# Kernel tuning notes

Hardware: AMD Instinct MI355X
Metric: run time of the kernel (lower is better)

Reference implementation:

```python
import jax, jax.numpy as jnp
import numpy as np

B, S, N = 1, 128, 256
C_IN, C_H, C_OUT = 256, 32, 128
EPS = 1e-5


def setup_inputs() -> dict:
    key = jax.random.key(0)
    k_m, k_wa, k_wb, k_wo = jax.random.split(key, 4)
    m = jax.random.normal(k_m, (B, S, N, C_IN), dtype=jnp.float32)
    mask = jnp.ones((B, S, N), dtype=jnp.float32)
    gamma = jnp.ones((C_IN,), dtype=jnp.float32)
    beta = jnp.zeros((C_IN,), dtype=jnp.float32)
    # nn.Linear weights are (out, in)
    Wa = jax.random.normal(k_wa, (C_H, C_IN), dtype=jnp.float32) / np.sqrt(C_IN).astype(np.float32)
    Wb = jax.random.normal(k_wb, (C_H, C_IN), dtype=jnp.float32) / np.sqrt(C_IN).astype(np.float32)
    # proj_o is final_init (zeros) in the source; use small random weights so the
    # baseline output is non-trivial for correctness checking.
    Wo = jax.random.normal(k_wo, (C_OUT, C_H * C_H), dtype=jnp.float32) / np.sqrt(C_H * C_H).astype(np.float32)
    bo = jnp.zeros((C_OUT,), dtype=jnp.float32)
    return {"m": m, "mask": mask, "gamma": gamma, "beta": beta,
            "Wa": Wa, "Wb": Wb, "Wo": Wo, "bo": bo}


def reference(m, mask, gamma, beta, Wa, Wb, Wo, bo):
    # LayerNorm over c_in
    mu = jnp.mean(m, axis=-1, keepdims=True)
    var = jnp.mean((m - mu) ** 2, axis=-1, keepdims=True)
    mn = (m - mu) * jax.lax.rsqrt(var + EPS) * gamma + beta  # (B,S,N,c_in)

    mk = mask[..., None]  # (B,S,N,1)
    a = jnp.einsum('bsni,hi->bsnh', mn, Wa) * mk  # (B,S,N,c_h)
    b = jnp.einsum('bsni,hi->bsnh', mn, Wb) * mk  # (B,S,N,c_h)

    # pairwise mask count over S, clamped to >= 1
    num_mask = jnp.clip(jnp.einsum('bsi,bsj->bij', mask, mask), 1.0, None)  # (B,N,N)

    # outer-product mean over the sequence dim
    z = jnp.einsum('bsic,bsjd->bijcd', a, b)  # (B,N,N,c_h,c_h)
    z = z.reshape(z.shape[0], z.shape[1], z.shape[2], C_H * C_H)
    z = z / num_mask[..., None]

    return jnp.einsum('bijk,ok->bijo', z, Wo) + bo  # (B,N,N,c_out)
```

## Files before the change

kernel.cpp:

```cpp
#include <hip/hip_runtime.h>
#include <hip/hip_bf16.h>

#define S_DIM 128
#define N_DIM 256
#define CIN   256
#define CH    32
#define COUT  128

typedef __attribute__((ext_vector_type(8))) short bf16x8;
typedef __attribute__((ext_vector_type(4))) float f32x4;
typedef __attribute__((ext_vector_type(16))) float f32x16;

__device__ __forceinline__ unsigned short f2bf(float f) {
  union { float f; unsigned int u; } v; v.f = f;
  unsigned int u = v.u;
  return (unsigned short)((u + 0x7FFFu + ((u >> 16) & 1u)) >> 16);
}

__device__ __forceinline__ unsigned int pk2(float x, float y) {
  float2 f2; f2.x = x; f2.y = y;
  __hip_bfloat162 h = __float22bfloat162_rn(f2);
  union { __hip_bfloat162 h; unsigned int u; } c; c.h = h;
  return c.u;
}

__global__ __launch_bounds__(256) void lnp_prep_kernel(
    const float* __restrict__ m, const float* __restrict__ mask,
    const float* __restrict__ gamma, const float* __restrict__ beta,
    const float* __restrict__ Wa, const float* __restrict__ Wb,
    const float* __restrict__ Wo,
    float* __restrict__ rnm, unsigned short* __restrict__ wo3,
    unsigned short* __restrict__ a_t, unsigned short* __restrict__ b_t) {
  const int b = blockIdx.x, t = threadIdx.x;
  if (b < 1024) {
    __shared__ __align__(16) unsigned short mn[32][264];
    __shared__ __align__(16) unsigned short wabs[64 * 256];
    const int i = b & 255, s0 = (b >> 8) * 32;
    const int w = t >> 6, l = t & 63, lq = l >> 4, lr = l & 15;

    #pragma unroll
    for (int it = 0; it < 8; it++) {
      const int gi = it * 256 + t;
      const int r = gi >> 5, g = gi & 31;
      const float* src = (r < 32) ? (Wa + r * 256 + g * 8)
                                  : (Wb + (r - 32) * 256 + g * 8);
      const int gp = (g & 16) | ((g ^ (r & 15)) & 15);
      unsigned short* dst = &wabs[r * 256 + gp * 8];
      const float4 v0 = *(const float4*)(src);
      const float4 v1 = *(const float4*)(src + 4);
      dst[0] = f2bf(v0.x); dst[1] = f2bf(v0.y); dst[2] = f2bf(v0.z); dst[3] = f2bf(v0.w);
      dst[4] = f2bf(v1.x); dst[5] = f2bf(v1.y); dst[6] = f2bf(v1.z); dst[7] = f2bf(v1.w);
    }

    const float4 g4 = *(const float4*)(gamma + l * 4);
    const float4 b4 = *(const float4*)(beta + l * 4);

    for (int rr = 0; rr < 8; rr++) {
      const int r = w * 8 + rr;
      const int s = s0 + r;
      const float4 v = *(const float4*)(m + ((size_t)(s * N_DIM + i)) * CIN + l * 4);
      float sum = v.x + v.y + v.z + v.w;
      float sq  = v.x * v.x + v.y * v.y + v.z * v.z + v.w * v.w;
      #pragma unroll
      for (int off = 32; off > 0; off >>= 1) {
        sum += __shfl_down(sum, off);
        sq  += __shfl_down(sq, off);
      }
      sum = __shfl(sum, 0); sq = __shfl(sq, 0);
      const float mu = sum * (1.0f / CIN);
      const float var = fmaxf(sq * (1.0f / CIN) - mu * mu, 0.0f);
      const float rs = rsqrtf(var + 1e-5f);
      const float mk = mask[s * N_DIM + i];
      ushort4 p;
      p.x = f2bf(((v.x - mu) * rs * g4.x + b4.x) * mk);
      p.y = f2bf(((v.y - mu) * rs * g4.y + b4.y) * mk);
      p.z = f2bf(((v.z - mu) * rs * g4.z + b4.z) * mk);
      p.w = f2bf(((v.w - mu) * rs * g4.w + b4.w) * mk);
      *(ushort4*)(&mn[r][l * 4]) = p;
    }
    __syncthreads();

    const int wm = w & 1;
    const int n2 = w >> 1;
    f32x4 acc0 = {0.f, 0.f, 0.f, 0.f}, acc1 = {0.f, 0.f, 0.f, 0.f};
    #pragma unroll
    for (int ks = 0; ks < 8; ks++) {
      const int k0 = ks * 32 + lq * 8;
      const int g = ks * 4 + lq;
      const int gp = (g & 16) | ((g ^ lr) & 15);
      const bf16x8 af = *(const bf16x8*)(&mn[wm * 16 + lr][k0]);
      const bf16x8 bf0 = *(const bf16x8*)(&wabs[(n2 * 32 + lr) * 256 + gp * 8]);
      const bf16x8 bf1 = *(const bf16x8*)(&wabs[(n2 * 32 + 16 + lr) * 256 + gp * 8]);
      acc0 = __builtin_amdgcn_mfma_f32_16x16x32_bf16(af, bf0, acc0, 0, 0, 0);
      acc1 = __builtin_amdgcn_mfma_f32_16x16x32_bf16(af, bf1, acc1, 0, 0, 0);
    }

    unsigned short* dst = (n2 == 0) ? a_t : b_t;
    const int scol = s0 + wm * 16 + lq * 4;
    ushort4 q0, q1;
    q0.x = f2bf(acc0[0]); q0.y = f2bf(acc0[1]); q0.z = f2bf(acc0[2]); q0.w = f2bf(acc0[3]);
    q1.x = f2bf(acc1[0]); q1.y = f2bf(acc1[1]); q1.z = f2bf(acc1[2]); q1.w = f2bf(acc1[3]);
    *(ushort4*)(dst + ((size_t)(i * CH + lr)) * S_DIM + scol) = q0;
    *(ushort4*)(dst + ((size_t)(i * CH + 16 + lr)) * S_DIM + scol) = q1;
  } else if (b < 1152) {
    const int r = b - 1024;
    #pragma unroll
    for (int q = 0; q < 4; q++) {
      const int f = r * 1024 + q * 256 + t;
      const int e = f & 7, l = (f >> 3) & 63;
      const int step = (f >> 9) & 63, og = f >> 15;
      const int kp = step * 16 + (l >> 5) * 8 + e;
      const int c = kp & 31, d = kp >> 5;
      const int o = og * 32 + (l & 31);
      wo3[f] = f2bf(Wo[o * 1024 + c * 32 + d]);
    }
  } else {
    const int i = b - 1152;
    float acc = 0.f;
    #pragma unroll 8
    for (int s = 0; s < S_DIM; s++)
      acc += mask[s * N_DIM + i] * mask[s * N_DIM + t];
    acc = fmaxf(acc, 1.0f);
    rnm[i * N_DIM + t] = 1.0f / acc;
  }
}

__global__ __launch_bounds__(1024, 4) void fused_kernel(
    const unsigned short* __restrict__ a_t, const unsigned short* __restrict__ b_t,
    const unsigned short* __restrict__ wo3, const float* __restrict__ rnm,
    const float* __restrict__ bo, float* __restrict__ out) {
  extern __shared__ __align__(16) unsigned short smem[];
  unsigned short* sA = smem;
  unsigned short* sB = smem + 32768;
  unsigned short* sZ = smem;

  const int t = threadIdx.x, w = t >> 6, l = t & 63;
  const int lq = l >> 4, lr = l & 15;
  const int bx = blockIdx.x, by = blockIdx.y;

  const unsigned short* srcA = a_t + (size_t)bx * 32768;
  const unsigned short* srcB = b_t + (size_t)by * 32768;
  #pragma unroll
  for (int it = 0; it < 4; it++) {
    const int idx = it * 1024 + t;
    const int r = idx >> 4, g = idx & 15;
    const int dst = r * 128 + ((g ^ (r & 15)) * 8);
    *(bf16x8*)(&sA[dst]) = *(const bf16x8*)(srcA + idx * 8);
    *(bf16x8*)(&sB[dst]) = *(const bf16x8*)(srcB + idx * 8);
  }
  __syncthreads();

  const int wy = (w >> 2) * 64, wx = (w & 3) * 64;
  f32x4 acc[4][4];
  #pragma unroll
  for (int a = 0; a < 4; a++)
    #pragma unroll
    for (int c = 0; c < 4; c++) acc[a][c] = (f32x4){0.f, 0.f, 0.f, 0.f};

  #pragma unroll
  for (int ks = 0; ks < 4; ks++) {
    const int g0 = ks * 4 + lq;
    bf16x8 afr[4], bfr[4];
    #pragma unroll
    for (int a = 0; a < 4; a++) {
      const int ra = wy + a * 16 + lr;
      afr[a] = *(const bf16x8*)(&sA[ra * 128 + ((g0 ^ (ra & 15)) * 8)]);
      const int rb = wx + a * 16 + lr;
      bfr[a] = *(const bf16x8*)(&sB[rb * 128 + ((g0 ^ (rb & 15)) * 8)]);
    }
    #pragma unroll
    for (int a = 0; a < 4; a++)
      #pragma unroll
      for (int c = 0; c < 4; c++)
        acc[a][c] = __builtin_amdgcn_mfma_f32_16x16x32_bf16(afr[a], bfr[c], acc[a][c], 0, 0, 0);
  }
  __syncthreads();

  #pragma unroll
  for (int a = 0; a < 4; a++) {
    #pragma unroll
    for (int c = 0; c < 4; c++) {
      const int zrb = wy + a * 16 + lq * 4;
      const int zc  = wx + c * 16 + lr;
      const int pair = (zrb >> 5) * 8 + (zc >> 5);
      const int off = (zc & 31) * 32 + (zrb & 31);
      const int g = off >> 3;
      const int gp = (g & ~7) | ((g ^ (g >> 3) ^ pair) & 7);
      uint2 q;
      q.x = pk2(acc[a][c][0], acc[a][c][1]);
      q.y = pk2(acc[a][c][2], acc[a][c][3]);
      *(uint2*)(&sZ[pair * 1024 + gp * 8 + (off & 7)]) = q;
    }
  }
  __syncthreads();

  const int ph = w & 1, og = (w >> 1) & 3, kh = w >> 3;
  const int pair2 = ph * 32 + (l & 31);
  const int zbase = pair2 * 1024;
  const unsigned short* wop =
      wo3 + ((size_t)(og * 64 + kh * 32) * 64 + l) * 8;
  f32x16 acc2;
  #pragma unroll
  for (int r = 0; r < 16; r++) acc2[r] = 0.f;

  #pragma unroll 8
  for (int j = 0; j < 32; j++) {
    const int s = kh * 32 + j;
    const int g = s * 2 + (l >> 5);
    const int gp = (g & ~7) | ((g ^ (g >> 3) ^ pair2) & 7);
    const bf16x8 zf = *(const bf16x8*)(&sZ[zbase + gp * 8]);
    const bf16x8 wf = *(const bf16x8*)(wop + j * 512);
    acc2 = __builtin_amdgcn_mfma_f32_32x32x16_bf16(zf, wf, acc2, 0, 0, 0);
  }
  __syncthreads();

  float* fpart = (float*)sZ;
  const int job = w & 7;
  if (kh) {
    #pragma unroll
    for (int r = 0; r < 16; r++)
      fpart[(job * 16 + r) * 64 + l] = acc2[r];
  }
  __syncthreads();

  if (!kh) {
    const int o = og * 32 + (l & 31);
    const float bov = bo[o];
    #pragma unroll
    for (int r = 0; r < 16; r++) {
      const int row = (r & 3) + 8 * (r >> 2) + 4 * (l >> 5);
      const int pr = ph * 32 + row;
      const int ii = bx * 8 + (pr >> 3);
      const int jj = by * 8 + (pr & 7);
      const float sc = rnm[ii * N_DIM + jj];
      out[((size_t)(ii * N_DIM + jj)) * COUT + o] =
          (acc2[r] + fpart[(job * 16 + r) * 64 + l]) * sc + bov;
    }
  }
}

extern "C" void kernel_launch(void* const* d_in, const int* in_sizes, int n_in,
                              void* d_out, int out_size, void* d_ws, size_t ws_size,
                              hipStream_t stream) {
  const float* m     = (const float*)d_in[0];
  const float* mask  = (const float*)d_in[1];
  const float* gamma = (const float*)d_in[2];
  const float* beta  = (const float*)d_in[3];
  const float* Wa    = (const float*)d_in[4];
  const float* Wb    = (const float*)d_in[5];
  const float* Wo    = (const float*)d_in[6];
  const float* bo    = (const float*)d_in[7];
  float* out = (float*)d_out;

  char* ws = (char*)d_ws;
  float*          rnm = (float*)(ws);
  unsigned short* wo3 = (unsigned short*)(ws + 262144);
  unsigned short* a_t = (unsigned short*)(ws + 524288);
  unsigned short* b_t = (unsigned short*)(ws + 2621440);

  hipFuncSetAttribute((const void*)fused_kernel,
                      hipFuncAttributeMaxDynamicSharedMemorySize, 131072);

  lnp_prep_kernel<<<1408, 256, 0, stream>>>(m, mask, gamma, beta, Wa, Wb, Wo,
                                            rnm, wo3, a_t, b_t);
  fused_kernel<<<dim3(32, 32), 1024, 131072, stream>>>(a_t, b_t, wo3, rnm, bo, out);
}
```

Before: 146.0 us.

## Make fused kernel persistent with register prefetch of next tile

Turns the 32x32 grid into a persistent 256-block kernel where each block processes four output tiles in sequence. The next tile's A/B inputs are prefetched into registers while the current tile's epilogue runs. The second GEMM is re-split so each wave handles two pair groups over a quarter of K, sharing each Wo fragment load across two MFMAs. The epilogue reduces partials through a swizzled LDS buffer and writes coalesced float4 outputs. This adds register pressure and lowers parallelism to one block per CU, in exchange for overlapping loads and reusing Wo reads.

```diff
diff --git a/kernel.cpp b/kernel.cpp
--- a/kernel.cpp
+++ b/kernel.cpp
@@ -133,109 +133,152 @@
   unsigned short* sA = smem;
   unsigned short* sB = smem + 32768;
   unsigned short* sZ = smem;
+  float* fpart = (float*)smem;
 
   const int t = threadIdx.x, w = t >> 6, l = t & 63;
   const int lq = l >> 4, lr = l & 15;
-  const int bx = blockIdx.x, by = blockIdx.y;
-
-  const unsigned short* srcA = a_t + (size_t)bx * 32768;
-  const unsigned short* srcB = b_t + (size_t)by * 32768;
-  #pragma unroll
-  for (int it = 0; it < 4; it++) {
-    const int idx = it * 1024 + t;
-    const int r = idx >> 4, g = idx & 15;
-    const int dst = r * 128 + ((g ^ (r & 15)) * 8);
-    *(bf16x8*)(&sA[dst]) = *(const bf16x8*)(srcA + idx * 8);
-    *(bf16x8*)(&sB[dst]) = *(const bf16x8*)(srcB + idx * 8);
+
+  const int pair = t >> 4;
+  const int ob   = (t & 15) * 8;
+  const float4 bo0 = *(const float4*)(bo + ob);
+  const float4 bo1 = *(const float4*)(bo + ob + 4);
+  const int opc = pair * 128 + (ob ^ ((pair & 3) << 3));
+
+  const int og = w & 3, kq = w >> 2;
+  const int pA = l & 31, pB = 32 + pA;
+  const unsigned short* wop =
+      wo3 + ((size_t)(og * 64 + kq * 16) * 64 + l) * 8;
+  const int oc = og * 32 + (l & 31);
+
+  int tt = blockIdx.x;
+
+  bf16x8 pfA[4], pfB[4];
+  {
+    const unsigned short* srcA = a_t + (size_t)(tt >> 5) * 32768;
+    const unsigned short* srcB = b_t + (size_t)(tt & 31) * 32768;
+    #pragma unroll
+    for (int it = 0; it < 4; it++) {
+      pfA[it] = *(const bf16x8*)(srcA + (it * 1024 + t) * 8);
+      pfB[it] = *(const bf16x8*)(srcB + (it * 1024 + t) * 8);
+    }
   }
-  __syncthreads();
-
-  const int wy = (w >> 2) * 64, wx = (w & 3) * 64;
-  f32x4 acc[4][4];
-  #pragma unroll
-  for (int a = 0; a < 4; a++)
-    #pragma unroll
-    for (int c = 0; c < 4; c++) acc[a][c] = (f32x4){0.f, 0.f, 0.f, 0.f};
-
-  #pragma unroll
-  for (int ks = 0; ks < 4; ks++) {
-    const int g0 = ks * 4 + lq;
-    bf16x8 afr[4], bfr[4];
-    #pragma unroll
-    for (int a = 0; a < 4; a++) {
-      const int ra = wy + a * 16 + lr;
-      afr[a] = *(const bf16x8*)(&sA[ra * 128 + ((g0 ^ (ra & 15)) * 8)]);
-      const int rb = wx + a * 16 + lr;
-      bfr[a] = *(const bf16x8*)(&sB[rb * 128 + ((g0 ^ (rb & 15)) * 8)]);
-    }
-    #pragma unroll
-    for (int a = 0; a < 4; a++)
-      #pragma unroll
-      for (int c = 0; c < 4; c++)
-        acc[a][c] = __builtin_amdgcn_mfma_f32_16x16x32_bf16(afr[a], bfr[c], acc[a][c], 0, 0, 0);
-  }
-  __syncthreads();
-
-  #pragma unroll
-  for (int a = 0; a < 4; a++) {
-    #pragma unroll
-    for (int c = 0; c < 4; c++) {
-      const int zrb = wy + a * 16 + lq * 4;
-      const int zc  = wx + c * 16 + lr;
-      const int pair = (zrb >> 5) * 8 + (zc >> 5);
-      const int off = (zc & 31) * 32 + (zrb & 31);
-      const int g = off >> 3;
-      const int gp = (g & ~7) | ((g ^ (g >> 3) ^ pair) & 7);
-      uint2 q;
-      q.x = pk2(acc[a][c][0], acc[a][c][1]);
-      q.y = pk2(acc[a][c][2], acc[a][c][3]);
-      *(uint2*)(&sZ[pair * 1024 + gp * 8 + (off & 7)]) = q;
-    }
-  }
-  __syncthreads();
-
-  const int ph = w & 1, og = (w >> 1) & 3, kh = w >> 3;
-  const int pair2 = ph * 32 + (l & 31);
-  const int zbase = pair2 * 1024;
-  const unsigned short* wop =
-      wo3 + ((size_t)(og * 64 + kh * 32) * 64 + l) * 8;
-  f32x16 acc2;
-  #pragma unroll
-  for (int r = 0; r < 16; r++) acc2[r] = 0.f;
-
-  #pragma unroll 8
-  for (int j = 0; j < 32; j++) {
-    const int s = kh * 32 + j;
-    const int g = s * 2 + (l >> 5);
-    const int gp = (g & ~7) | ((g ^ (g >> 3) ^ pair2) & 7);
-    const bf16x8 zf = *(const bf16x8*)(&sZ[zbase + gp * 8]);
-    const bf16x8 wf = *(const bf16x8*)(wop + j * 512);
-    acc2 = __builtin_amdgcn_mfma_f32_32x32x16_bf16(zf, wf, acc2, 0, 0, 0);
-  }
-  __syncthreads();
-
-  float* fpart = (float*)sZ;
-  const int job = w & 7;
-  if (kh) {
-    #pragma unroll
-    for (int r = 0; r < 16; r++)
-      fpart[(job * 16 + r) * 64 + l] = acc2[r];
-  }
-  __syncthreads();
-
-  if (!kh) {
-    const int o = og * 32 + (l & 31);
-    const float bov = bo[o];
-    #pragma unroll
-    for (int r = 0; r < 16; r++) {
-      const int row = (r & 3) + 8 * (r >> 2) + 4 * (l >> 5);
-      const int pr = ph * 32 + row;
-      const int ii = bx * 8 + (pr >> 3);
-      const int jj = by * 8 + (pr & 7);
-      const float sc = rnm[ii * N_DIM + jj];
-      out[((size_t)(ii * N_DIM + jj)) * COUT + o] =
-          (acc2[r] + fpart[(job * 16 + r) * 64 + l]) * sc + bov;
-    }
+
+  #pragma unroll 1
+  for (int rep = 0; rep < 4; ++rep) {
+    const int bx = tt >> 5, by = tt & 31;
+
+    #pragma unroll
+    for (int it = 0; it < 4; it++) {
+      const int idx = it * 1024 + t;
+      const int rw = idx >> 4, g = idx & 15;
+      const int dst = rw * 128 + ((g ^ (rw & 15)) * 8);
+      *(bf16x8*)(&sA[dst]) = pfA[it];
+      *(bf16x8*)(&sB[dst]) = pfB[it];
+    }
+    __syncthreads();
+
+    const int wy = (w >> 2) * 64, wx = (w & 3) * 64;
+    f32x4 acc[4][4];
+    #pragma unroll
+    for (int a2 = 0; a2 < 4; a2++)
+      #pragma unroll
+      for (int c2 = 0; c2 < 4; c2++) acc[a2][c2] = (f32x4){0.f, 0.f, 0.f, 0.f};
+
+    #pragma unroll
+    for (int ks = 0; ks < 4; ks++) {
+      const int g0 = ks * 4 + lq;
+      bf16x8 afr[4], bfr[4];
+      #pragma unroll
+      for (int a2 = 0; a2 < 4; a2++) {
+        const int ra = wy + a2 * 16 + lr;
+        afr[a2] = *(const bf16x8*)(&sA[ra * 128 + ((g0 ^ (ra & 15)) * 8)]);
+        const int rb = wx + a2 * 16 + lr;
+        bfr[a2] = *(const bf16x8*)(&sB[rb * 128 + ((g0 ^ (rb & 15)) * 8)]);
+      }
+      #pragma unroll
+      for (int a2 = 0; a2 < 4; a2++)
+        #pragma unroll
+        for (int c2 = 0; c2 < 4; c2++)
+          acc[a2][c2] = __builtin_amdgcn_mfma_f32_16x16x32_bf16(afr[a2], bfr[c2], acc[a2][c2], 0, 0, 0);
+    }
+    __syncthreads();
+
+    #pragma unroll
+    for (int a2 = 0; a2 < 4; a2++) {
+      #pragma unroll
+      for (int c2 = 0; c2 < 4; c2++) {
+        const int zrb = wy + a2 * 16 + lq * 4;
+        const int zc  = wx + c2 * 16 + lr;
+        const int pr = (zrb >> 5) * 8 + (zc >> 5);
+        const int off = (zc & 31) * 32 + (zrb & 31);
+        const int g = off >> 3;
+        const int gp = (g & ~7) | ((g ^ (g >> 3) ^ pr) & 7);
+        uint2 q;
+        q.x = pk2(acc[a2][c2][0], acc[a2][c2][1]);
+        q.y = pk2(acc[a2][c2][2], acc[a2][c2][3]);
+        *(uint2*)(&sZ[pr * 1024 + gp * 8 + (off & 7)]) = q;
+      }
+    }
+    __syncthreads();
+
+    f32x16 accA, accB;
+    #pragma unroll
+    for (int q2 = 0; q2 < 16; q2++) { accA[q2] = 0.f; accB[q2] = 0.f; }
+
+    #pragma unroll 8
+    for (int j = 0; j < 16; j++) {
+      const int s = kq * 16 + j;
+      const int g = s * 2 + (l >> 5);
+      const int gA = (g & ~7) | ((g ^ (g >> 3) ^ pA) & 7);
+      const int gB = (g & ~7) | ((g ^ (g >> 3) ^ pB) & 7);
+      const bf16x8 zfA = *(const bf16x8*)(&sZ[pA * 1024 + gA * 8]);
+      const bf16x8 zfB = *(const bf16x8*)(&sZ[pB * 1024 + gB * 8]);
+      const bf16x8 wf = *(const bf16x8*)(wop + (size_t)j * 512);
+      accA = __builtin_amdgcn_mfma_f32_32x32x16_bf16(zfA, wf, accA, 0, 0, 0);
+      accB = __builtin_amdgcn_mfma_f32_32x32x16_bf16(zfB, wf, accB, 0, 0, 0);
+    }
+    __syncthreads();
+
+    #pragma unroll
+    for (int q2 = 0; q2 < 16; q2++) {
+      const int row = (q2 & 3) + 8 * (q2 >> 2) + 4 * (l >> 5);
+      const int xo = oc ^ ((q2 & 3) << 3);
+      fpart[kq * 8192 + row * 128 + xo] = accA[q2];
+      fpart[kq * 8192 + (row + 32) * 128 + xo] = accB[q2];
+    }
+    __syncthreads();
+
+    const int ii = bx * 8 + (pair >> 3), jj = by * 8 + (pair & 7);
+    const float sc = rnm[ii * N_DIM + jj];
+
+    if (rep < 3) {
+      const int ntt = tt + 256;
+      const unsigned short* srcA = a_t + (size_t)(ntt >> 5) * 32768;
+      const unsigned short* srcB = b_t + (size_t)(ntt & 31) * 32768;
+      #pragma unroll
+      for (int it = 0; it < 4; it++) {
+        pfA[it] = *(const bf16x8*)(srcA + (it * 1024 + t) * 8);
+        pfB[it] = *(const bf16x8*)(srcB + (it * 1024 + t) * 8);
+      }
+    }
+
+    f32x4 u0 = {0.f, 0.f, 0.f, 0.f}, u1 = {0.f, 0.f, 0.f, 0.f};
+    #pragma unroll
+    for (int q2 = 0; q2 < 4; q2++) {
+      u0 += *(const f32x4*)(&fpart[q2 * 8192 + opc]);
+      u1 += *(const f32x4*)(&fpart[q2 * 8192 + opc + 4]);
+    }
+    float* po = out + ((size_t)(ii * N_DIM + jj)) * COUT + ob;
+    float4 w0, w1;
+    w0.x = u0[0] * sc + bo0.x; w0.y = u0[1] * sc + bo0.y;
+    w0.z = u0[2] * sc + bo0.z; w0.w = u0[3] * sc + bo0.w;
+    w1.x = u1[0] * sc + bo1.x; w1.y = u1[1] * sc + bo1.y;
+    w1.z = u1[2] * sc + bo1.z; w1.w = u1[3] * sc + bo1.w;
+    *(float4*)(po)     = w0;
+    *(float4*)(po + 4) = w1;
+    __syncthreads();
+
+    tt += 256;
   }
 }
 
@@ -263,5 +306,5 @@
 
   lnp_prep_kernel<<<1408, 256, 0, stream>>>(m, mask, gamma, beta, Wa, Wb, Wo,
                                             rnm, wo3, a_t, b_t);
-  fused_kernel<<<dim3(32, 32), 1024, 131072, stream>>>(a_t, b_t, wo3, rnm, bo, out);
-}
+  fused_kernel<<<256, 1024, 131072, stream>>>(a_t, b_t, wo3, rnm, bo, out);
+}
```

Measured after the change: 219.6 us. +50.3%, slower.

## Split Wo projection K four ways, reuse Wo fragments across pair halves, vectorize output

Applied to the files above, without the earlier changes.

Each wave now handles both pair halves (two accumulators) for one output group and a quarter of the K dimension. This reuses every Wo fragment load for two MFMAs instead of one. The four K-partials are written to shared memory with an XOR swizzle and reduced by all threads. Each thread then writes 8 contiguous output floats with float4 stores, replacing 16 scattered scalar stores per lane from only half the waves. The cost is more shared memory traffic for the partial reduction and twice the accumulator registers.

```diff
diff --git a/kernel.cpp b/kernel.cpp
--- a/kernel.cpp
+++ b/kernel.cpp
@@ -133,6 +133,7 @@
   unsigned short* sA = smem;
   unsigned short* sB = smem + 32768;
   unsigned short* sZ = smem;
+  float* fpart = (float*)smem;
 
   const int t = threadIdx.x, w = t >> 6, l = t & 63;
   const int lq = l >> 4, lr = l & 15;
@@ -182,61 +183,73 @@
     for (int c = 0; c < 4; c++) {
       const int zrb = wy + a * 16 + lq * 4;
       const int zc  = wx + c * 16 + lr;
-      const int pair = (zrb >> 5) * 8 + (zc >> 5);
+      const int pr = (zrb >> 5) * 8 + (zc >> 5);
       const int off = (zc & 31) * 32 + (zrb & 31);
       const int g = off >> 3;
-      const int gp = (g & ~7) | ((g ^ (g >> 3) ^ pair) & 7);
+      const int gp = (g & ~7) | ((g ^ (g >> 3) ^ pr) & 7);
       uint2 q;
       q.x = pk2(acc[a][c][0], acc[a][c][1]);
       q.y = pk2(acc[a][c][2], acc[a][c][3]);
-      *(uint2*)(&sZ[pair * 1024 + gp * 8 + (off & 7)]) = q;
-    }
-  }
-  __syncthreads();
-
-  const int ph = w & 1, og = (w >> 1) & 3, kh = w >> 3;
-  const int pair2 = ph * 32 + (l & 31);
-  const int zbase = pair2 * 1024;
+      *(uint2*)(&sZ[pr * 1024 + gp * 8 + (off & 7)]) = q;
+    }
+  }
+  __syncthreads();
+
+  const int og = w & 3, kq = w >> 2;
+  const int pA = l & 31, pB = 32 + pA;
   const unsigned short* wop =
-      wo3 + ((size_t)(og * 64 + kh * 32) * 64 + l) * 8;
-  f32x16 acc2;
-  #pragma unroll
-  for (int r = 0; r < 16; r++) acc2[r] = 0.f;
+      wo3 + ((size_t)(og * 64 + kq * 16) * 64 + l) * 8;
+  f32x16 accA, accB;
+  #pragma unroll
+  for (int r = 0; r < 16; r++) { accA[r] = 0.f; accB[r] = 0.f; }
 
   #pragma unroll 8
-  for (int j = 0; j < 32; j++) {
-    const int s = kh * 32 + j;
+  for (int j = 0; j < 16; j++) {
+    const int s = kq * 16 + j;
     const int g = s * 2 + (l >> 5);
-    const int gp = (g & ~7) | ((g ^ (g >> 3) ^ pair2) & 7);
-    const bf16x8 zf = *(const bf16x8*)(&sZ[zbase + gp * 8]);
-    const bf16x8 wf = *(const bf16x8*)(wop + j * 512);
-    acc2 = __builtin_amdgcn_mfma_f32_32x32x16_bf16(zf, wf, acc2, 0, 0, 0);
-  }
-  __syncthreads();
-
-  float* fpart = (float*)sZ;
-  const int job = w & 7;
-  if (kh) {
-    #pragma unroll
-    for (int r = 0; r < 16; r++)
-      fpart[(job * 16 + r) * 64 + l] = acc2[r];
-  }
-  __syncthreads();
-
-  if (!kh) {
-    const int o = og * 32 + (l & 31);
-    const float bov = bo[o];
-    #pragma unroll
-    for (int r = 0; r < 16; r++) {
-      const int row = (r & 3) + 8 * (r >> 2) + 4 * (l >> 5);
-      const int pr = ph * 32 + row;
-      const int ii = bx * 8 + (pr >> 3);
-      const int jj = by * 8 + (pr & 7);
-      const float sc = rnm[ii * N_DIM + jj];
-      out[((size_t)(ii * N_DIM + jj)) * COUT + o] =
-          (acc2[r] + fpart[(job * 16 + r) * 64 + l]) * sc + bov;
-    }
-  }
+    const int gA = (g & ~7) | ((g ^ (g >> 3) ^ pA) & 7);
+    const int gB = (g & ~7) | ((g ^ (g >> 3) ^ pB) & 7);
+    const bf16x8 zfA = *(const bf16x8*)(&sZ[pA * 1024 + gA * 8]);
+    const bf16x8 zfB = *(const bf16x8*)(&sZ[pB * 1024 + gB * 8]);
+    const bf16x8 wf = *(const bf16x8*)(wop + (size_t)j * 512);
+    accA = __builtin_amdgcn_mfma_f32_32x32x16_bf16(zfA, wf, accA, 0, 0, 0);
+    accB = __builtin_amdgcn_mfma_f32_32x32x16_bf16(zfB, wf, accB, 0, 0, 0);
+  }
+  __syncthreads();
+
+  const int oc = og * 32 + (l & 31);
+  #pragma unroll
+  for (int r = 0; r < 16; r++) {
+    const int row = (r & 3) + 8 * (r >> 2) + 4 * (l >> 5);
+    const int xo = oc ^ ((r & 3) << 3);
+    fpart[kq * 8192 + row * 128 + xo] = accA[r];
+    fpart[kq * 8192 + (row + 32) * 128 + xo] = accB[r];
+  }
+  __syncthreads();
+
+  const int pair = t >> 4;
+  const int ob   = (t & 15) * 8;
+  const float4 bo0 = *(const float4*)(bo + ob);
+  const float4 bo1 = *(const float4*)(bo + ob + 4);
+  const int opc = pair * 128 + (ob ^ ((pair & 3) << 3));
+
+  const int ii = bx * 8 + (pair >> 3), jj = by * 8 + (pair & 7);
+  const float sc = rnm[ii * N_DIM + jj];
+
+  f32x4 u0 = {0.f, 0.f, 0.f, 0.f}, u1 = {0.f, 0.f, 0.f, 0.f};
+  #pragma unroll
+  for (int q = 0; q < 4; q++) {
+    u0 += *(const f32x4*)(&fpart[q * 8192 + opc]);
+    u1 += *(const f32x4*)(&fpart[q * 8192 + opc + 4]);
+  }
+  float* po = out + ((size_t)(ii * N_DIM + jj)) * COUT + ob;
+  float4 w0, w1;
+  w0.x = u0[0] * sc + bo0.x; w0.y = u0[1] * sc + bo0.y;
+  w0.z = u0[2] * sc + bo0.z; w0.w = u0[3] * sc + bo0.w;
+  w1.x = u1[0] * sc + bo1.x; w1.y = u1[1] * sc + bo1.y;
+  w1.z = u1[2] * sc + bo1.z; w1.w = u1[3] * sc + bo1.w;
+  *(float4*)(po)     = w0;
+  *(float4*)(po + 4) = w1;
 }
 
 extern "C" void kernel_launch(void* const* d_in, const int* in_sizes, int n_in,
```

Result: slower. 151.7 us (+3.9%).
